# Kernel optimization log

Measured on AMD Instinct MI355X. Metric: run time of the kernel, lower is better.

Reference implementation:

```python
import jax, jax.numpy as jnp
import numpy as np


def setup_inputs() -> dict:
    key = jax.random.key(0)
    k1, k2 = jax.random.split(key)
    B, C, H, W = 64, 1280, 32, 32
    NUM_WINDS = 8
    x = jax.random.normal(k1, (B, C, H, W), dtype=jnp.float32)
    wind_indices = jax.random.randint(k2, (B,), 0, NUM_WINDS)
    wind_weights = jnp.ones((NUM_WINDS,), dtype=jnp.float32)
    return {"x": x, "wind_indices": wind_indices, "wind_weights": wind_weights}


def reference(x, wind_indices, wind_weights):
    # Global average pool over H, W -> [B, C]
    pooled = jnp.mean(x, axis=(2, 3))
    # Softmax over wind weights, gather per-sample scale -> [B, 1]
    weights = jax.nn.softmax(wind_weights, axis=0)
    scale = weights[wind_indices][:, None]
    return pooled * scale
```

## Files before the change

kernel.cpp:

```cpp
#include <hip/hip_runtime.h>
#include <hip/hip_bf16.h>


#define NUM_WINDS 8
#define C_DIM 1280
#define HW 1024

__global__ __launch_bounds__(256) void wind_pool_kernel(
    const float* __restrict__ x,
    const int* __restrict__ wind_indices,
    const float* __restrict__ wind_weights,
    float* __restrict__ out,
    int n_rows) {
    const int gtid = blockIdx.x * blockDim.x + threadIdx.x;
    const int wave_id = gtid >> 6;
    const int lane = gtid & 63;
    if (wave_id >= n_rows) return;

    const float4* row = reinterpret_cast<const float4*>(x + (size_t)wave_id * HW);
    float4 v0 = row[lane];
    float4 v1 = row[lane + 64];
    float4 v2 = row[lane + 128];
    float4 v3 = row[lane + 192];

    float s = (v0.x + v0.y) + (v0.z + v0.w)
            + (v1.x + v1.y) + (v1.z + v1.w)
            + (v2.x + v2.y) + (v2.z + v2.w)
            + (v3.x + v3.y) + (v3.z + v3.w);

    #pragma unroll
    for (int off = 32; off > 0; off >>= 1)
        s += __shfl_down(s, off, 64);

    if (lane == 0) {
        const int b = wave_id / C_DIM;
        const int idx = wind_indices[b];
        float w[NUM_WINDS];
        float m = -1e30f;
        #pragma unroll
        for (int i = 0; i < NUM_WINDS; ++i) {
            w[i] = wind_weights[i];
            m = fmaxf(m, w[i]);
        }
        float denom = 0.0f;
        #pragma unroll
        for (int i = 0; i < NUM_WINDS; ++i)
            denom += __expf(w[i] - m);
        const float scale = __expf(w[idx] - m) / denom;
        out[wave_id] = s * (1.0f / (float)HW) * scale;
    }
}

extern "C" void kernel_launch(void* const* d_in, const int* in_sizes, int n_in,
                              void* d_out, int out_size, void* d_ws, size_t ws_size,
                              hipStream_t stream) {
    const float* x = (const float*)d_in[0];
    const int* wind_indices = (const int*)d_in[1];
    const float* wind_weights = (const float*)d_in[2];
    float* out = (float*)d_out;

    const int n_rows = out_size;
    const int waves_per_block = 256 / 64;
    const int n_blocks = (n_rows + waves_per_block - 1) / waves_per_block;

    wind_pool_kernel<<<n_blocks, 256, 0, stream>>>(x, wind_indices, wind_weights, out, n_rows);
}
```

Measured before the change: 430.7 us.

## Process two rows per wave with nontemporal vector loads

Each wave now reduces two adjacent rows instead of one, issuing eight 16-byte loads per lane and interleaving the two shuffle reductions. All loads use nontemporal hints, since the input is streamed once. The launch uses half as many waves. Both rows share one batch index, which holds because C is even, but an odd row count would be mishandled.

```diff
diff --git a/kernel.cpp b/kernel.cpp
--- a/kernel.cpp
+++ b/kernel.cpp
@@ -5,6 +5,9 @@
 #define NUM_WINDS 8
 #define C_DIM 1280
 #define HW 1024
+#define ROW_F4 256
+
+typedef float f32x4 __attribute__((ext_vector_type(4)));
 
 __global__ __launch_bounds__(256) void wind_pool_kernel(
     const float* __restrict__ x,
@@ -15,25 +18,38 @@
     const int gtid = blockIdx.x * blockDim.x + threadIdx.x;
     const int wave_id = gtid >> 6;
     const int lane = gtid & 63;
-    if (wave_id >= n_rows) return;
+    const int r0 = wave_id * 2;
+    if (r0 >= n_rows) return;
 
-    const float4* row = reinterpret_cast<const float4*>(x + (size_t)wave_id * HW);
-    float4 v0 = row[lane];
-    float4 v1 = row[lane + 64];
-    float4 v2 = row[lane + 128];
-    float4 v3 = row[lane + 192];
+    const f32x4* row0 = reinterpret_cast<const f32x4*>(x) + (size_t)r0 * ROW_F4;
+    const f32x4* row1 = row0 + ROW_F4;
 
-    float s = (v0.x + v0.y) + (v0.z + v0.w)
-            + (v1.x + v1.y) + (v1.z + v1.w)
-            + (v2.x + v2.y) + (v2.z + v2.w)
-            + (v3.x + v3.y) + (v3.z + v3.w);
+    f32x4 a0 = __builtin_nontemporal_load(row0 + lane);
+    f32x4 a1 = __builtin_nontemporal_load(row0 + lane + 64);
+    f32x4 a2 = __builtin_nontemporal_load(row0 + lane + 128);
+    f32x4 a3 = __builtin_nontemporal_load(row0 + lane + 192);
+    f32x4 b0 = __builtin_nontemporal_load(row1 + lane);
+    f32x4 b1 = __builtin_nontemporal_load(row1 + lane + 64);
+    f32x4 b2 = __builtin_nontemporal_load(row1 + lane + 128);
+    f32x4 b3 = __builtin_nontemporal_load(row1 + lane + 192);
+
+    float s0 = (a0.x + a0.y) + (a0.z + a0.w)
+             + (a1.x + a1.y) + (a1.z + a1.w)
+             + (a2.x + a2.y) + (a2.z + a2.w)
+             + (a3.x + a3.y) + (a3.z + a3.w);
+    float s1 = (b0.x + b0.y) + (b0.z + b0.w)
+             + (b1.x + b1.y) + (b1.z + b1.w)
+             + (b2.x + b2.y) + (b2.z + b2.w)
+             + (b3.x + b3.y) + (b3.z + b3.w);
 
     #pragma unroll
-    for (int off = 32; off > 0; off >>= 1)
-        s += __shfl_down(s, off, 64);
+    for (int off = 32; off > 0; off >>= 1) {
+        s0 += __shfl_down(s0, off, 64);
+        s1 += __shfl_down(s1, off, 64);
+    }
 
     if (lane == 0) {
-        const int b = wave_id / C_DIM;
+        const int b = r0 / C_DIM;
         const int idx = wind_indices[b];
         float w[NUM_WINDS];
         float m = -1e30f;
@@ -46,8 +62,9 @@
         #pragma unroll
         for (int i = 0; i < NUM_WINDS; ++i)
             denom += __expf(w[i] - m);
-        const float scale = __expf(w[idx] - m) / denom;
-        out[wave_id] = s * (1.0f / (float)HW) * scale;
+        const float scale = __expf(w[idx] - m) / denom * (1.0f / (float)HW);
+        out[r0] = s0 * scale;
+        out[r0 + 1] = s1 * scale;
     }
 }
 
@@ -60,8 +77,9 @@
     float* out = (float*)d_out;
 
     const int n_rows = out_size;
+    const int n_waves = n_rows / 2;
     const int waves_per_block = 256 / 64;
-    const int n_blocks = (n_rows + waves_per_block - 1) / waves_per_block;
+    const int n_blocks = (n_waves + waves_per_block - 1) / waves_per_block;
 
     wind_pool_kernel<<<n_blocks, 256, 0, stream>>>(x, wind_indices, wind_weights, out, n_rows);
 }
```

After: 406.9 us. 1.06x faster.
